# Performance work log

Measured on AMD Instinct MI355X. Metric: run time of the kernel, lower is better.

The kernel has to match this reference:

```python
import jax, jax.numpy as jnp
import numpy as np

P = 64        # num_particles
H = 256       # hidden_dim
E = 64        # input_size
B = 32        # batch
S = 128       # seq_len
ALPHA = 0.1   # soft-resampling alpha


def setup_inputs() -> dict:
    key = jax.random.key(0)
    ks = jax.random.split(key, 8)
    sc = 0.05
    return {
        "observations": jax.random.normal(ks[0], (B, S, E), jnp.float32),
        "h0": jax.random.uniform(ks[1], (B * P, H), jnp.float32),
        "c0": jax.random.uniform(ks[2], (B * P, H), jnp.float32),
        "W_ih": jax.random.normal(ks[3], (4 * H, E), jnp.float32) * sc,
        "b_ih": jnp.zeros((4 * H,), jnp.float32),
        "W_hh": jax.random.normal(ks[4], (4 * H, H), jnp.float32) * sc,
        "b_hh": jnp.zeros((4 * H,), jnp.float32),
        "W_obs": jax.random.normal(ks[5], (1, H + E), jnp.float32) * sc,
        "b_obs": jnp.zeros((1,), jnp.float32),
        "W_out": jax.random.normal(ks[6], (1, H), jnp.float32) * sc,
        "b_out": jnp.zeros((1,), jnp.float32),
    }


def _log_softmax_particles(p):
    # p: (P*B, 1), particle-major flatten of (P, B); normalize over particle axis
    return jax.nn.log_softmax(p.reshape(P, -1, 1), axis=0).reshape(-1, 1)


def _soft_resample(key, h, c, p):
    # soft resampling: q = alpha*w + (1-alpha)/P, sample indices, reweight
    nB = p.shape[0] // P
    w = ALPHA * jnp.exp(p) + (1.0 - ALPHA) / P                 # (P*B, 1)
    logits = jnp.log(w.reshape(P, nB).T)                       # (B, P)
    idx = jax.random.categorical(key, logits, axis=-1, shape=(P, nB))  # (P, B)
    flat = (idx * nB + jnp.arange(nB)[None, :]).reshape(-1)    # particle-major gather ids
    h_new, c_new = h[flat], c[flat]
    w_new = ALPHA * jnp.exp(p.reshape(-1)[flat]) + (1.0 - ALPHA) / P
    p_new = _log_softmax_particles(jnp.log(w_new)[:, None])
    return h_new, c_new, p_new


def _forward(observations, h0, c0, W_ih, b_ih, W_hh, b_hh, W_obs, b_obs, W_out, b_out):
    emb = jnp.tile(observations, (P, 1, 1))       # (P*B, S, E) particle-major
    xs = jnp.swapaxes(emb, 0, 1)                  # (S, P*B, E)
    p0 = jnp.full((B * P, 1), np.log(1.0 / P), jnp.float32)
    key0 = jax.random.key(42)

    def step(carry, x_t):
        h, c, p, key = carry
        key, sub = jax.random.split(key)
        gates = x_t @ W_ih.T + b_ih + h @ W_hh.T + b_hh        # (P*B, 4H)
        i, f, g, o = jnp.split(gates, 4, axis=1)
        c1 = jax.nn.sigmoid(f) * c + jax.nn.sigmoid(i) * jnp.tanh(g)
        h1 = jax.nn.sigmoid(o) * jnp.tanh(c1)
        # per-particle observation log-likelihood
        logp_obs = jnp.concatenate([x_t, h1], axis=1) @ W_obs.T + b_obs  # (P*B, 1)
        p1 = _log_softmax_particles(logp_obs + p)
        h1, c1, p1 = _soft_resample(sub, h1, c1, p1)
        return (h1, c1, p1, key), (h1, p1)

    _, (hs, ps) = jax.lax.scan(step, (h0, c0, p0, key0), xs)
    # hs: (S, P*B, H); ps: (S, P*B, 1)
    y = jnp.sum(hs.reshape(S, P, B, H) * jnp.exp(ps.reshape(S, P, B, 1)), axis=1)  # (S, B, H)
    y_out = jax.nn.leaky_relu(y @ W_out.T + b_out)           # (S, B, 1)
    pf_out = jax.nn.leaky_relu(hs @ W_out.T + b_out)         # (S, P*B, 1)
    return y_out, pf_out


def reference(observations, h0, c0, W_ih, b_ih, W_hh, b_hh, W_obs, b_obs, W_out, b_out):
    return _forward(observations, h0, c0, W_ih, b_ih, W_hh, b_hh, W_obs, b_obs, W_out, b_out)
```

## Files before the change

kernel.cpp:

```cpp
#include <hip/hip_runtime.h>
#include <stdint.h>

#define NPART 64
#define NBATCH 32
#define NSEQ 128
#define NEIN 64
#define NHID 256

__device__ __forceinline__ uint32_t rotl32(uint32_t x, uint32_t d) {
  return (x << d) | (x >> (32u - d));
}

__device__ __forceinline__ void threefry2x32(uint32_t k0, uint32_t k1,
                                             uint32_t& x0, uint32_t& x1) {
  uint32_t k2 = k0 ^ k1 ^ 0x1BD11BDAu;
  x0 += k0; x1 += k1;
#define TFR(r) { x0 += x1; x1 = rotl32(x1, r); x1 ^= x0; }
  TFR(13u) TFR(15u) TFR(26u) TFR(6u)
  x0 += k1; x1 += k2 + 1u;
  TFR(17u) TFR(29u) TFR(16u) TFR(24u)
  x0 += k2; x1 += k0 + 2u;
  TFR(13u) TFR(15u) TFR(26u) TFR(6u)
  x0 += k0; x1 += k1 + 3u;
  TFR(17u) TFR(29u) TFR(16u) TFR(24u)
  x0 += k1; x1 += k2 + 4u;
  TFR(13u) TFR(15u) TFR(26u) TFR(6u)
  x0 += k2; x1 += k0 + 5u;
#undef TFR
}

__device__ __forceinline__ float lreluf(float x) { return x >= 0.f ? x : 0.01f * x; }

__global__ void k_prep(const float* __restrict__ h0, const float* __restrict__ c0,
                       const float* __restrict__ W_ih, const float* __restrict__ W_hh,
                       float* __restrict__ hA, float* __restrict__ cA,
                       float4* __restrict__ Wih4, float4* __restrict__ Whh4,
                       float* __restrict__ p_cur, float* __restrict__ y_acc,
                       int* __restrict__ idx_buf, uint2* __restrict__ subs) {
  int tid = blockIdx.x * blockDim.x + threadIdx.x;
  int nthr = gridDim.x * blockDim.x;
  for (int i = tid; i < NPART * NBATCH * NHID; i += nthr) {
    hA[i] = h0[i];
    cA[i] = c0[i];
  }
  for (int i = tid; i < NEIN * NHID; i += nthr) {
    int e = i >> 8, j = i & 255;
    Wih4[i] = make_float4(W_ih[j * NEIN + e], W_ih[(256 + j) * NEIN + e],
                          W_ih[(512 + j) * NEIN + e], W_ih[(768 + j) * NEIN + e]);
  }
  for (int i = tid; i < NHID * NHID; i += nthr) {
    int k = i >> 8, j = i & 255;
    Whh4[i] = make_float4(W_hh[j * NHID + k], W_hh[(256 + j) * NHID + k],
                          W_hh[(512 + j) * NHID + k], W_hh[(768 + j) * NHID + k]);
  }
  for (int i = tid; i < NPART * NBATCH; i += nthr) {
    p_cur[i] = -4.1588830833596715f;
    idx_buf[i] = i >> 5;
  }
  for (int i = tid; i < NBATCH; i += nthr) y_acc[i] = 0.f;
  if (tid < NSEQ) {
    uint32_t k0u = 0u, k1u = 42u, sx = 0u, sy = 0u;
    for (int i = 0; i <= tid; ++i) {
      uint32_t s0 = 0u, s1 = 1u; threefry2x32(k0u, k1u, s0, s1);
      uint32_t n0 = 0u, n1 = 0u; threefry2x32(k0u, k1u, n0, n1);
      sx = s0; sy = s1; k0u = n0; k1u = n1;
    }
    subs[tid] = make_uint2(sx, sy);
  }
}

__global__ __launch_bounds__(256, 2)
void k_step(int t,
            const float* __restrict__ h_prev, const float* __restrict__ c_prev,
            float* __restrict__ h_out, float* __restrict__ c_out,
            const int* __restrict__ idx_buf, const float* __restrict__ obs,
            const float4* __restrict__ Wih4, const float4* __restrict__ Whh4,
            const float* __restrict__ b_ih, const float* __restrict__ b_hh,
            float* __restrict__ y_acc, const float* __restrict__ b_out_p,
            float* __restrict__ d_out) {
  __shared__ float4 Wbuf[32 * 64];
  __shared__ float h_s[16][NHID];
  __shared__ float obs_s[NEIN];
  __shared__ int src_s[16];
  const int tid = threadIdx.x;
  const int cb = blockIdx.x;
  const int rb = blockIdx.y;
  const int b = rb >> 2;
  const int qg = rb & 3;

  if (t > 0 && cb == 0 && rb == 0 && tid < NBATCH) {
    d_out[(t - 1) * NBATCH + tid] = lreluf(y_acc[tid] + b_out_p[0]);
    y_acc[tid] = 0.f;
  }

  if (tid < NEIN) obs_s[tid] = obs[(b * NSEQ + t) * NEIN + tid];
  if (tid < 16) {
    int q = qg * 16 + tid;
    src_s[tid] = idx_buf[q * NBATCH + b] * NBATCH + b;
  }
  __syncthreads();
  for (int i = tid; i < 16 * (NHID / 4); i += 256) {
    int r = i >> 6, kq = i & 63;
    ((float4*)h_s[r])[kq] = ((const float4*)(h_prev + src_s[r] * NHID))[kq];
  }
  __syncthreads();

  const int jloc = tid & 63;
  const int rg = tid >> 6;
  const int jglob = cb * 64 + jloc;

  float xb[4];
  {
    float4 w0 = make_float4(b_ih[jglob] + b_hh[jglob],
                            b_ih[jglob + 256] + b_hh[jglob + 256],
                            b_ih[jglob + 512] + b_hh[jglob + 512],
                            b_ih[jglob + 768] + b_hh[jglob + 768]);
    xb[0] = w0.x; xb[1] = w0.y; xb[2] = w0.z; xb[3] = w0.w;
  }
#pragma unroll 8
  for (int e = 0; e < NEIN; ++e) {
    float xv = obs_s[e];
    float4 w = Wih4[e * NHID + jglob];
    xb[0] += xv * w.x;
    xb[1] += xv * w.y;
    xb[2] += xv * w.z;
    xb[3] += xv * w.w;
  }

  float acc[4][4];
#pragma unroll
  for (int rr = 0; rr < 4; ++rr)
#pragma unroll
    for (int g = 0; g < 4; ++g) acc[rr][g] = 0.f;

  const float4* hrow4[4];
#pragma unroll
  for (int rr = 0; rr < 4; ++rr) hrow4[rr] = (const float4*)h_s[rg * 4 + rr];

  for (int c = 0; c < 8; ++c) {
    const int k0 = c * 32;
    __syncthreads();
    for (int i = tid; i < 32 * 64; i += 256)
      Wbuf[i] = Whh4[(k0 + (i >> 6)) * NHID + cb * 64 + (i & 63)];
    __syncthreads();
#pragma unroll
    for (int k4 = 0; k4 < 8; ++k4) {
      float4 h4[4];
#pragma unroll
      for (int rr = 0; rr < 4; ++rr) h4[rr] = hrow4[rr][(k0 >> 2) + k4];
#pragma unroll
      for (int kk = 0; kk < 4; ++kk) {
        float4 w = Wbuf[(k4 * 4 + kk) * 64 + jloc];
#pragma unroll
        for (int rr = 0; rr < 4; ++rr) {
          float hv = ((const float*)&h4[rr])[kk];
          acc[rr][0] += hv * w.x;
          acc[rr][1] += hv * w.y;
          acc[rr][2] += hv * w.z;
          acc[rr][3] += hv * w.w;
        }
      }
    }
  }

#pragma unroll
  for (int rr = 0; rr < 4; ++rr) {
    int q = qg * 16 + rg * 4 + rr;
    int n = q * NBATCH + b;
    float iv = acc[rr][0] + xb[0];
    float fv = acc[rr][1] + xb[1];
    float gv = acc[rr][2] + xb[2];
    float ov = acc[rr][3] + xb[3];
    float cp = c_prev[src_s[rg * 4 + rr] * NHID + jglob];
    float si = 1.f / (1.f + expf(-iv));
    float sf = 1.f / (1.f + expf(-fv));
    float so = 1.f / (1.f + expf(-ov));
    float c1 = sf * cp + si * tanhf(gv);
    float h1 = so * tanhf(c1);
    h_out[n * NHID + jglob] = h1;
    c_out[n * NHID + jglob] = c1;
  }
}

__global__ __launch_bounds__(512)
void k_pf(int t, const float* __restrict__ obs, const float* __restrict__ W_obs,
          const float* __restrict__ b_obs_p, const float* __restrict__ h1,
          float* __restrict__ p_cur, int* __restrict__ idx_buf,
          const uint2* __restrict__ subs, const float* __restrict__ W_out,
          const float* __restrict__ b_out_p, float* __restrict__ y_acc,
          float* __restrict__ d_out) {
  __shared__ float logp_s[NPART], p1_s[NPART], lg_s[NPART], pdot_s[NPART];
  __shared__ int idx_s[NPART];
  __shared__ float lx_s;
  const int tid = threadIdx.x;
  const int lane = tid & 63;
  const int wv = tid >> 6;
  const int b = blockIdx.x;

  float Wo[4], Wu[4];
#pragma unroll
  for (int m = 0; m < 4; ++m) {
    Wo[m] = W_obs[NEIN + m * 64 + lane];
    Wu[m] = W_out[m * 64 + lane];
  }
  if (wv == 0) {
    float v = obs[(b * NSEQ + t) * NEIN + lane] * W_obs[lane];
#pragma unroll
    for (int off = 32; off > 0; off >>= 1) v += __shfl_down(v, off, 64);
    if (lane == 0) lx_s = v + b_obs_p[0];
  }
  {
    float hv[8][4];
#pragma unroll
    for (int u = 0; u < 8; ++u) {
      const float* hr = h1 + ((wv * 8 + u) * NBATCH + b) * NHID;
#pragma unroll
      for (int m = 0; m < 4; ++m) hv[u][m] = hr[m * 64 + lane];
    }
#pragma unroll
    for (int u = 0; u < 8; ++u) {
      float hp = 0.f;
#pragma unroll
      for (int m = 0; m < 4; ++m) hp += hv[u][m] * Wo[m];
#pragma unroll
      for (int off = 32; off > 0; off >>= 1) hp += __shfl_down(hp, off, 64);
      if (lane == 0) logp_s[wv * 8 + u] = hp;
    }
#pragma unroll
    for (int u = 0; u < 8; ++u) {
      float pd = 0.f;
#pragma unroll
      for (int m = 0; m < 4; ++m) pd += hv[u][m] * Wu[m];
#pragma unroll
      for (int off = 32; off > 0; off >>= 1) pd += __shfl_down(pd, off, 64);
      if (lane == 0) pdot_s[wv * 8 + u] = pd;
    }
  }
  __syncthreads();

  if (wv == 0) {
    int n = lane * NBATCH + b;
    float x = logp_s[lane] + lx_s + p_cur[n];
    float m = x;
#pragma unroll
    for (int off = 32; off > 0; off >>= 1) {
      float o = __shfl_xor(m, off, 64);
      m = o > m ? o : m;
    }
    float s = expf(x - m);
#pragma unroll
    for (int off = 32; off > 0; off >>= 1) s += __shfl_xor(s, off, 64);
    float p1 = x - m - logf(s);
    p1_s[lane] = p1;
    lg_s[lane] = logf(0.1f * expf(p1) + 0.9f / 64.f);
  }
  __syncthreads();

  const uint2 sub = subs[t];
  {
    float v[8]; int id[8];
#pragma unroll
    for (int u = 0; u < 8; ++u) {
      int q = wv * 8 + u;
      uint32_t x0 = 0u;
      uint32_t x1 = (uint32_t)((q * NBATCH + b) * NPART + lane);
      threefry2x32(sub.x, sub.y, x0, x1);
      uint32_t bits = x0 ^ x1;
      uint32_t mant = bits >> 9;
      float uu = (mant == 0u) ? 1.17549435e-38f
                              : (float)mant * 1.1920928955078125e-07f;
      float g = -logf(-logf(uu));
      v[u] = g + lg_s[lane];
      id[u] = lane;
    }
#pragma unroll
    for (int off = 32; off > 0; off >>= 1) {
#pragma unroll
      for (int u = 0; u < 8; ++u) {
        float ov = __shfl_xor(v[u], off, 64);
        int oi = __shfl_xor(id[u], off, 64);
        if (ov > v[u] || (ov == v[u] && oi < id[u])) { v[u] = ov; id[u] = oi; }
      }
    }
    if (lane == 0) {
#pragma unroll
      for (int u = 0; u < 8; ++u) idx_s[wv * 8 + u] = id[u];
    }
  }
  __syncthreads();

  if (wv == 0) {
    int src = idx_s[lane];
    int n = lane * NBATCH + b;
    idx_buf[n] = src;
    float wn = 0.1f * expf(p1_s[src]) + 0.9f / 64.f;
    float lw = logf(wn);
    float m = lw;
#pragma unroll
    for (int off = 32; off > 0; off >>= 1) {
      float o = __shfl_xor(m, off, 64);
      m = o > m ? o : m;
    }
    float s = expf(lw - m);
#pragma unroll
    for (int off = 32; off > 0; off >>= 1) s += __shfl_xor(s, off, 64);
    float pn = lw - m - logf(s);
    p_cur[n] = pn;
    float pd = pdot_s[src];
    d_out[NSEQ * NBATCH + t * (NPART * NBATCH) + lane * NBATCH + b] =
        lreluf(pd + b_out_p[0]);
    float yv = expf(pn) * pd;
#pragma unroll
    for (int off = 32; off > 0; off >>= 1) yv += __shfl_down(yv, off, 64);
    if (lane == 0) y_acc[b] += yv;
  }
}

__global__ void k_final(const float* __restrict__ y_acc,
                        const float* __restrict__ b_out_p, float* __restrict__ d_out) {
  int b = threadIdx.x;
  if (b < NBATCH) {
    d_out[(NSEQ - 1) * NBATCH + b] = lreluf(y_acc[b] + b_out_p[0]);
  }
}

extern "C" void kernel_launch(void* const* d_in, const int* in_sizes, int n_in,
                              void* d_out, int out_size, void* d_ws, size_t ws_size,
                              hipStream_t stream) {
  const float* obs   = (const float*)d_in[0];
  const float* h0    = (const float*)d_in[1];
  const float* c0    = (const float*)d_in[2];
  const float* W_ih  = (const float*)d_in[3];
  const float* b_ih  = (const float*)d_in[4];
  const float* W_hh  = (const float*)d_in[5];
  const float* b_hh  = (const float*)d_in[6];
  const float* W_obs = (const float*)d_in[7];
  const float* b_obs = (const float*)d_in[8];
  const float* W_out = (const float*)d_in[9];
  const float* b_out = (const float*)d_in[10];
  float* out = (float*)d_out;

  char* w = (char*)d_ws;
  const size_t state = (size_t)NPART * NBATCH * NHID * sizeof(float);
  float* hA = (float*)w;        w += state;
  float* hB = (float*)w;        w += state;
  float* cA = (float*)w;        w += state;
  float* cB = (float*)w;        w += state;
  float* p_cur = (float*)w;     w += NPART * NBATCH * sizeof(float);
  float* y_acc = (float*)w;     w += NBATCH * sizeof(float);
  uint2* subs = (uint2*)w;      w += NSEQ * sizeof(uint2);
  float4* Wih4 = (float4*)w;    w += NEIN * NHID * sizeof(float4);
  float4* Whh4 = (float4*)w;    w += NHID * NHID * sizeof(float4);
  int* idx_buf = (int*)w;       w += NPART * NBATCH * sizeof(int);

  k_prep<<<dim3(256), dim3(256), 0, stream>>>(h0, c0, W_ih, W_hh, hA, cA, Wih4, Whh4,
                                              p_cur, y_acc, idx_buf, subs);
  for (int t = 0; t < NSEQ; ++t) {
    const float* hp = (t & 1) ? hB : hA;
    float* hn       = (t & 1) ? hA : hB;
    const float* cp = (t & 1) ? cB : cA;
    float* cn       = (t & 1) ? cA : cB;
    k_step<<<dim3(4, 128), dim3(256), 0, stream>>>(
        t, hp, cp, hn, cn, idx_buf, obs, Wih4, Whh4, b_ih, b_hh, y_acc, b_out, out);
    k_pf<<<dim3(NBATCH), dim3(512), 0, stream>>>(
        t, obs, W_obs, b_obs, hn, p_cur, idx_buf, subs, W_out, b_out, y_acc, out);
  }
  k_final<<<dim3(1), dim3(64), 0, stream>>>(y_acc, b_out, out);
}
```

Measured before the change: 5.799 ms.

## Double-buffer W_hh tiles and read gathered h rows directly from global

The LSTM step kernel now handles 32 particles per block instead of 16, halving the grid to 4x64 blocks and doubling the reuse of each W_hh tile held in shared memory. W_hh is streamed in 16-row chunks through a two-buffer shared memory scheme: the next chunk is prefetched into registers while the current one is consumed, which cuts the number of barriers. The h staging in shared memory is removed, and each wave reads its 8 gathered h rows straight from global memory via wave-uniform pointers. In exchange, register use grows (8x4 accumulators), the launch bound drops to one block per SM, and the GPU has fewer blocks to fill it.

Result: slower. 8.809 ms (+51.9%).

```diff
diff --git a/kernel.cpp b/kernel.cpp
--- a/kernel.cpp
+++ b/kernel.cpp
@@ -69,7 +69,7 @@
   }
 }
 
-__global__ __launch_bounds__(256, 2)
+__global__ __launch_bounds__(256, 1)
 void k_step(int t,
             const float* __restrict__ h_prev, const float* __restrict__ c_prev,
             float* __restrict__ h_out, float* __restrict__ c_out,
@@ -78,15 +78,16 @@
             const float* __restrict__ b_ih, const float* __restrict__ b_hh,
             float* __restrict__ y_acc, const float* __restrict__ b_out_p,
             float* __restrict__ d_out) {
-  __shared__ float4 Wbuf[32 * 64];
-  __shared__ float h_s[16][NHID];
+  __shared__ float4 Wbuf[2][16 * 64];
   __shared__ float obs_s[NEIN];
-  __shared__ int src_s[16];
+  __shared__ int src_s[32];
   const int tid = threadIdx.x;
+  const int lane = tid & 63;
+  const int wv = tid >> 6;
   const int cb = blockIdx.x;
   const int rb = blockIdx.y;
-  const int b = rb >> 2;
-  const int qg = rb & 3;
+  const int b = rb >> 1;
+  const int qh = rb & 1;
 
   if (t > 0 && cb == 0 && rb == 0 && tid < NBATCH) {
     d_out[(t - 1) * NBATCH + tid] = lreluf(y_acc[tid] + b_out_p[0]);
@@ -94,20 +95,25 @@
   }
 
   if (tid < NEIN) obs_s[tid] = obs[(b * NSEQ + t) * NEIN + tid];
-  if (tid < 16) {
-    int q = qg * 16 + tid;
+  if (tid < 32) {
+    int q = qh * 32 + tid;
     src_s[tid] = idx_buf[q * NBATCH + b] * NBATCH + b;
   }
   __syncthreads();
-  for (int i = tid; i < 16 * (NHID / 4); i += 256) {
-    int r = i >> 6, kq = i & 63;
-    ((float4*)h_s[r])[kq] = ((const float4*)(h_prev + src_s[r] * NHID))[kq];
-  }
-  __syncthreads();
-
-  const int jloc = tid & 63;
-  const int rg = tid >> 6;
-  const int jglob = cb * 64 + jloc;
+
+  const int jglob = cb * 64 + lane;
+
+#define LOADR(wr, ch)                                                         \
+  _Pragma("unroll")                                                           \
+  for (int it = 0; it < 4; ++it)                                              \
+    wr[it] = Whh4[((ch) * 16 + it * 4 + wv) * NHID + cb * 64 + lane];
+#define WRITER(wr, nb)                                                        \
+  _Pragma("unroll")                                                           \
+  for (int it = 0; it < 4; ++it)                                              \
+    Wbuf[nb][(it * 4 + wv) * 64 + lane] = wr[it];
+
+  float4 wr0[4];
+  LOADR(wr0, 0);
 
   float xb[4];
   {
@@ -127,32 +133,38 @@
     xb[3] += xv * w.w;
   }
 
-  float acc[4][4];
-#pragma unroll
-  for (int rr = 0; rr < 4; ++rr)
+  int srcs[8];
+  const float4* hq[8];
+#pragma unroll
+  for (int rr = 0; rr < 8; ++rr) {
+    int s = __builtin_amdgcn_readfirstlane(src_s[wv * 8 + rr]);
+    srcs[rr] = s;
+    hq[rr] = (const float4*)(h_prev + (size_t)s * NHID);
+  }
+
+  float acc[8][4];
+#pragma unroll
+  for (int rr = 0; rr < 8; ++rr)
 #pragma unroll
     for (int g = 0; g < 4; ++g) acc[rr][g] = 0.f;
 
-  const float4* hrow4[4];
-#pragma unroll
-  for (int rr = 0; rr < 4; ++rr) hrow4[rr] = (const float4*)h_s[rg * 4 + rr];
-
-  for (int c = 0; c < 8; ++c) {
-    const int k0 = c * 32;
-    __syncthreads();
-    for (int i = tid; i < 32 * 64; i += 256)
-      Wbuf[i] = Whh4[(k0 + (i >> 6)) * NHID + cb * 64 + (i & 63)];
-    __syncthreads();
-#pragma unroll
-    for (int k4 = 0; k4 < 8; ++k4) {
-      float4 h4[4];
-#pragma unroll
-      for (int rr = 0; rr < 4; ++rr) h4[rr] = hrow4[rr][(k0 >> 2) + k4];
+  WRITER(wr0, 0);
+  __syncthreads();
+
+  for (int ch = 0; ch < 16; ++ch) {
+    const int nb = ch & 1;
+    float4 wr[4];
+    if (ch < 15) { LOADR(wr, ch + 1); }
+#pragma unroll
+    for (int k4 = 0; k4 < 4; ++k4) {
+      float4 h4[8];
+#pragma unroll
+      for (int rr = 0; rr < 8; ++rr) h4[rr] = hq[rr][ch * 4 + k4];
 #pragma unroll
       for (int kk = 0; kk < 4; ++kk) {
-        float4 w = Wbuf[(k4 * 4 + kk) * 64 + jloc];
-#pragma unroll
-        for (int rr = 0; rr < 4; ++rr) {
+        float4 w = Wbuf[nb][(k4 * 4 + kk) * 64 + lane];
+#pragma unroll
+        for (int rr = 0; rr < 8; ++rr) {
           float hv = ((const float*)&h4[rr])[kk];
           acc[rr][0] += hv * w.x;
           acc[rr][1] += hv * w.y;
@@ -161,17 +173,21 @@
         }
       }
     }
-  }
-
-#pragma unroll
-  for (int rr = 0; rr < 4; ++rr) {
-    int q = qg * 16 + rg * 4 + rr;
+    if (ch < 15) { WRITER(wr, nb ^ 1); }
+    __syncthreads();
+  }
+#undef LOADR
+#undef WRITER
+
+#pragma unroll
+  for (int rr = 0; rr < 8; ++rr) {
+    int q = qh * 32 + wv * 8 + rr;
     int n = q * NBATCH + b;
     float iv = acc[rr][0] + xb[0];
     float fv = acc[rr][1] + xb[1];
     float gv = acc[rr][2] + xb[2];
     float ov = acc[rr][3] + xb[3];
-    float cp = c_prev[src_s[rg * 4 + rr] * NHID + jglob];
+    float cp = c_prev[srcs[rr] * NHID + jglob];
     float si = 1.f / (1.f + expf(-iv));
     float sf = 1.f / (1.f + expf(-fv));
     float so = 1.f / (1.f + expf(-ov));
@@ -360,7 +376,7 @@
     float* hn       = (t & 1) ? hA : hB;
     const float* cp = (t & 1) ? cB : cA;
     float* cn       = (t & 1) ? cA : cB;
-    k_step<<<dim3(4, 128), dim3(256), 0, stream>>>(
+    k_step<<<dim3(4, 64), dim3(256), 0, stream>>>(
         t, hp, cp, hn, cn, idx_buf, obs, Wih4, Whh4, b_ih, b_hh, y_acc, b_out, out);
     k_pf<<<dim3(NBATCH), dim3(512), 0, stream>>>(
         t, obs, W_obs, b_obs, hn, p_cur, idx_buf, subs, W_out, b_out, y_acc, out);
```
